# Kernel optimization log

Measured on AMD Instinct MI355X. Metric: run time of the kernel, lower is better.

Reference implementation:

```python
import jax, jax.numpy as jnp
import numpy as np

B, N, D = 2048, 128, 32   # samples, features, per-feature embed dim
H = 8                     # num_head
ND = N * D                # flattened width = 4096
U = D * N // H            # per-head units = 512
DH = D // H               # per-head output feature dim = 4


def setup_inputs() -> dict:
    key = jax.random.key(0)
    k_x, k_q, k_k, k_v, k_o = jax.random.split(key, 5)
    scale_w = 0.02  # keep QK^T logits in a sane range for softmax
    x = jax.random.normal(k_x, (B, N, D), dtype=jnp.float32)
    Wq = jax.random.normal(k_q, (H, ND, U), dtype=jnp.float32) * scale_w
    Wk = jax.random.normal(k_k, (H, ND, U), dtype=jnp.float32) * scale_w
    Wv = jax.random.normal(k_v, (H, ND, U), dtype=jnp.float32) * scale_w
    Wo = jax.random.normal(k_o, (D, D), dtype=jnp.float32) * (1.0 / np.sqrt(D))
    return {"x": x, "Wq": Wq, "Wk": Wk, "Wv": Wv, "Wo": Wo}


def reference(x, Wq, Wk, Wv, Wo):
    b, n, d = x.shape
    scale = d ** (-0.5)          # note: original scales by feature dim d, not head dim
    xf = x.reshape(b, n * d)     # (b, nd); the leading 1 axis in TF is vacuous
    # Batched per-head projections (collapses the Python head loop into one GEMM each)
    q = jnp.einsum('bf,hfu->hbu', xf, Wq)   # (H, b, U)
    k = jnp.einsum('bf,hfu->hbu', xf, Wk)   # (H, b, U)
    v = jnp.einsum('bf,hfu->hbu', xf, Wv)   # (H, b, U)
    scores = jax.nn.softmax(jnp.einsum('hbu,hcu->hbc', q, k) * scale, axis=-1)  # (H, b, b)
    av = jnp.einsum('hbc,hcu->hbu', scores, v)              # (H, b, U)
    # per-head reshape (b, U) -> (b, n, d/H), then concat heads along last dim
    av = av.reshape(H, b, n, d // H)                         # (H, b, n, dh)
    concat = jnp.transpose(av, (1, 2, 0, 3)).reshape(b, n, d)  # (b, n, d)
    return concat @ Wo  # dropout rate is 0 -> identity
```

## Files before the change

kernel.cpp:

```cpp
#include <hip/hip_runtime.h>
#include <stdint.h>
#include <math.h>

typedef short    s16x8 __attribute__((ext_vector_type(8)));
typedef float    f32x4 __attribute__((ext_vector_type(4)));
typedef uint32_t u32x4 __attribute__((ext_vector_type(4)));
typedef unsigned short u16x4 __attribute__((ext_vector_type(4)));

__device__ __forceinline__ uint16_t f2bf(float f) {
  union { float f; uint32_t u; } v; v.f = f;
  uint32_t r = v.u + 0x7fffu + ((v.u >> 16) & 1u);
  return (uint16_t)(r >> 16);
}
__device__ __forceinline__ float bf2f(uint16_t h) {
  union { uint32_t u; float f; } v; v.u = ((uint32_t)h) << 16;
  return v.f;
}

__device__ __forceinline__ void gld16(const void* g, void* l) {
  __builtin_amdgcn_global_load_lds(
      (const __attribute__((address_space(1))) void*)g,
      (__attribute__((address_space(3))) void*)l, 16, 0, 0);
}

__global__ __launch_bounds__(256) void cvt_x(const float* __restrict__ x,
                                             uint16_t* __restrict__ xf,
                                             float* __restrict__ rs) {
  if (blockIdx.x < 64) rs[blockIdx.x * 256 + threadIdx.x] = 0.f;
  size_t i = ((size_t)blockIdx.x * 256 + threadIdx.x) * 4;
  f32x4 v = *(const f32x4*)(x + i);
  u16x4 o = { f2bf(v.x), f2bf(v.y), f2bf(v.z), f2bf(v.w) };
  *(u16x4*)(xf + i) = o;
}

__global__ __launch_bounds__(256) void wtrans(const float* __restrict__ W0,
                                              const float* __restrict__ W1,
                                              const float* __restrict__ W2,
                                              uint16_t* __restrict__ Wt) {
  const int z = blockIdx.z;
  const float* W = (z < 8 ? W0 : (z < 16 ? W1 : W2)) + (size_t)(z & 7) * (4096 * 512);
  const int f0 = blockIdx.x * 32, u0 = blockIdx.y * 32;
  __shared__ float t[32][33];
  const int tid = threadIdx.x;
  {
    const int fi = tid >> 3, uu = (tid & 7) * 4;
    f32x4 v = *(const f32x4*)(W + (size_t)(f0 + fi) * 512 + u0 + uu);
    t[fi][uu] = v.x; t[fi][uu + 1] = v.y; t[fi][uu + 2] = v.z; t[fi][uu + 3] = v.w;
  }
  __syncthreads();
  {
    const int ui = tid >> 3, ff = (tid & 7) * 4;
    u16x4 o = { f2bf(t[ff][ui]), f2bf(t[ff + 1][ui]),
                f2bf(t[ff + 2][ui]), f2bf(t[ff + 3][ui]) };
    *(u16x4*)&Wt[((size_t)z * 512 + u0 + ui) * 4096 + f0 + ff] = o;
  }
}

template <int MODE>
__global__ __launch_bounds__(256, 4) void gemm_bt(
    const uint16_t* __restrict__ A, size_t sAz,
    const uint16_t* __restrict__ B, size_t sBz,
    void* __restrict__ C0, void* __restrict__ C1,
    int K, float scale, float* __restrict__ rs) {
  const int tid = threadIdx.x;
  const int wave = tid >> 6, lane = tid & 63;
  const int quad = lane >> 4, l16 = lane & 15;
  const int wrow = (wave >> 1) * 64, wcol = (wave & 1) * 64;
  const int m0 = blockIdx.y * 128, n0 = blockIdx.x * 128;
  const int z = blockIdx.z;
  A += (size_t)z * sAz;
  B += (size_t)z * sBz;

  __shared__ __align__(16) uint16_t lA[128 * 64];
  __shared__ __align__(16) uint16_t lB[128 * 64];

  f32x4 acc[4][4];
#pragma unroll
  for (int i = 0; i < 4; i++)
#pragma unroll
    for (int j = 0; j < 4; j++) acc[i][j] = f32x4{0.f, 0.f, 0.f, 0.f};

  const int lrow = lane >> 3;
  const int cs = ((lane & 7) ^ (lrow & 7)) * 8;
  const int rs0 = wave * 8;
  const uint16_t* gA = A + (size_t)(m0 + rs0 + lrow) * K + cs;
  const uint16_t* gB = B + (size_t)(n0 + rs0 + lrow) * K + cs;
  const size_t row32 = (size_t)32 * K;
  uint16_t* sA = &lA[rs0 * 64];
  uint16_t* sB = &lB[rs0 * 64];

  for (int k0 = 0; k0 < K; k0 += 64) {
    __syncthreads();
#pragma unroll
    for (int g = 0; g < 4; g++) {
      gld16(gA + g * row32, sA + g * 2048);
      gld16(gB + g * row32, sB + g * 2048);
    }
    gA += 64; gB += 64;
    __syncthreads();
#pragma unroll
    for (int h = 0; h < 2; h++) {
      s16x8 af[4], bfr[4];
      const int fsw = (((h * 4 + quad) ^ (l16 & 7)) * 8);
#pragma unroll
      for (int i = 0; i < 4; i++)
        af[i] = *(const s16x8*)&lA[(wrow + i * 16 + l16) * 64 + fsw];
#pragma unroll
      for (int j = 0; j < 4; j++)
        bfr[j] = *(const s16x8*)&lB[(wcol + j * 16 + l16) * 64 + fsw];
#pragma unroll
      for (int i = 0; i < 4; i++)
#pragma unroll
        for (int j = 0; j < 4; j++)
          acc[i][j] = __builtin_amdgcn_mfma_f32_16x16x32_bf16(af[i], bfr[j], acc[i][j], 0, 0, 0);
    }
  }

  const int mb = m0 + wrow + quad * 4;
  const int nb = n0 + wcol + l16;
  if (MODE == 4) {
    if (z < 16) {
      uint16_t* C = (uint16_t*)C0 + ((size_t)z << 20);
#pragma unroll
      for (int i = 0; i < 4; i++)
#pragma unroll
        for (int j = 0; j < 4; j++)
#pragma unroll
          for (int r = 0; r < 4; r++)
            C[(size_t)(mb + i * 16 + r) * 512 + (nb + j * 16)] = f2bf(acc[i][j][r]);
    } else {
      uint16_t* C = (uint16_t*)C1 + ((size_t)(z - 16) << 20);
#pragma unroll
      for (int i = 0; i < 4; i++)
#pragma unroll
        for (int j = 0; j < 4; j++) {
          u16x4 o = { f2bf(acc[i][j][0]), f2bf(acc[i][j][1]),
                      f2bf(acc[i][j][2]), f2bf(acc[i][j][3]) };
          *(u16x4*)&((uint16_t*)C)[(size_t)(nb + j * 16) * 2048 + (mb + i * 16)] = o;
        }
    }
  } else if (MODE == 2) {
    uint16_t* C = (uint16_t*)C0 + ((size_t)z << 22);
    float* rz = rs + (z << 11);
    float si[4][4];
#pragma unroll
    for (int i = 0; i < 4; i++)
#pragma unroll
      for (int r = 0; r < 4; r++) si[i][r] = 0.f;
#pragma unroll
    for (int i = 0; i < 4; i++)
#pragma unroll
      for (int j = 0; j < 4; j++)
#pragma unroll
        for (int r = 0; r < 4; r++) {
          float e = exp2f(fmaf(acc[i][j][r], scale, -43.2808512f));
          uint16_t hb = f2bf(e);
          C[(size_t)(mb + i * 16 + r) * 2048 + (nb + j * 16)] = hb;
          si[i][r] += bf2f(hb);
        }
#pragma unroll
    for (int i = 0; i < 4; i++)
#pragma unroll
      for (int r = 0; r < 4; r++) {
        float s = si[i][r];
        s += __shfl_xor(s, 1);
        s += __shfl_xor(s, 2);
        s += __shfl_xor(s, 4);
        s += __shfl_xor(s, 8);
        si[i][r] = s;
      }
    if (l16 == 0) {
#pragma unroll
      for (int i = 0; i < 4; i++)
#pragma unroll
        for (int r = 0; r < 4; r++)
          atomicAdd(&rz[mb + i * 16 + r], si[i][r]);
    }
  } else {
    float* C = (float*)C0 + ((size_t)z << 20);
    const float* rz = rs + (z << 11);
#pragma unroll
    for (int i = 0; i < 4; i++)
#pragma unroll
      for (int r = 0; r < 4; r++) {
        float w = 1.0f / rz[mb + i * 16 + r];
#pragma unroll
        for (int j = 0; j < 4; j++)
          C[(size_t)(mb + i * 16 + r) * 512 + (nb + j * 16)] = acc[i][j][r] * w;
      }
  }
}

__global__ __launch_bounds__(256) void out_proj(const float* __restrict__ av,
                                                const float* __restrict__ Wo,
                                                float* __restrict__ out) {
  __shared__ float lw[1024];
  const int tid = threadIdx.x;
#pragma unroll
  for (int i = 0; i < 4; i++) lw[tid + i * 256] = Wo[tid + i * 256];
  __syncthreads();
  const int p = blockIdx.x * 256 + tid;
  const int b = p >> 7, n = p & 127;
  float c[32];
#pragma unroll
  for (int h = 0; h < 8; h++) {
    f32x4 v = *(const f32x4*)(av + ((size_t)h * 2048 + b) * 512 + n * 4);
    c[h * 4] = v.x; c[h * 4 + 1] = v.y; c[h * 4 + 2] = v.z; c[h * 4 + 3] = v.w;
  }
  float o[32];
#pragma unroll
  for (int d = 0; d < 32; d++) o[d] = 0.f;
#pragma unroll
  for (int j = 0; j < 32; j++) {
    float cj = c[j];
#pragma unroll
    for (int d = 0; d < 32; d++) o[d] = fmaf(cj, lw[j * 32 + d], o[d]);
  }
  float* dst = out + (size_t)p * 32;
#pragma unroll
  for (int i = 0; i < 8; i++) {
    f32x4 v = { o[i * 4], o[i * 4 + 1], o[i * 4 + 2], o[i * 4 + 3] };
    *(f32x4*)(dst + i * 4) = v;
  }
}

extern "C" void kernel_launch(void* const* d_in, const int* in_sizes, int n_in,
                              void* d_out, int out_size, void* d_ws, size_t ws_size,
                              hipStream_t stream) {
  const float* x  = (const float*)d_in[0];
  const float* Wq = (const float*)d_in[1];
  const float* Wk = (const float*)d_in[2];
  const float* Wv = (const float*)d_in[3];
  const float* Wo = (const float*)d_in[4];
  float* out = (float*)d_out;

  uint8_t* ws = (uint8_t*)d_ws;
  uint16_t* Wt = (uint16_t*)(ws);
  uint16_t* P  = (uint16_t*)(ws);
  float*    av = (float*)(ws + 67108864);
  uint16_t* xf = (uint16_t*)(ws + 100663296);
  uint16_t* q  = (uint16_t*)(ws + 117440512);
  uint16_t* vt = (uint16_t*)(ws + 150994944);
  float*    rs = (float*)(ws + 167772160);

  const size_t WtH = (size_t)512 * 4096;
  const float scale2 = 0.17677669529663687f * 1.4426950408889634f;

  cvt_x<<<8192, 256, 0, stream>>>(x, xf, rs);
  wtrans<<<dim3(128, 16, 24), 256, 0, stream>>>(Wq, Wk, Wv, Wt);

  gemm_bt<4><<<dim3(4, 16, 24), 256, 0, stream>>>(
      xf, 0, Wt, WtH, q, vt, 4096, 0.f, nullptr);

  gemm_bt<2><<<dim3(16, 16, 8), 256, 0, stream>>>(
      q, (size_t)2048 * 512, q + (size_t)8 * 2048 * 512, (size_t)2048 * 512,
      P, nullptr, 512, scale2, rs);

  gemm_bt<3><<<dim3(4, 16, 8), 256, 0, stream>>>(
      P, (size_t)2048 * 2048, vt, (size_t)512 * 2048,
      av, nullptr, 2048, 0.f, rs);

  out_proj<<<1024, 256, 0, stream>>>(av, Wo, out);
}
```

Before: 572.1 us.

## Split-K the attention-value GEMM and widen weight transpose tiles

The P·V GEMM is split into two K halves across a doubled grid, and each half writes its own fp32 partial output. out_proj sums the two partials before the output projection. This raises block count and occupancy for a GEMM that previously launched too few blocks to fill the device, at the cost of an extra 32MB partial buffer read. The weight transpose kernel also processes 64x32 tiles with 8-wide bf16 stores to cut launch count and widen memory transactions.

Result: no change. 565.1 us (-1.2%).

```diff
diff --git a/kernel.cpp b/kernel.cpp
--- a/kernel.cpp
+++ b/kernel.cpp
@@ -6,6 +6,7 @@
 typedef float    f32x4 __attribute__((ext_vector_type(4)));
 typedef uint32_t u32x4 __attribute__((ext_vector_type(4)));
 typedef unsigned short u16x4 __attribute__((ext_vector_type(4)));
+typedef unsigned short u16x8 __attribute__((ext_vector_type(8)));
 
 __device__ __forceinline__ uint16_t f2bf(float f) {
   union { float f; uint32_t u; } v; v.f = f;
@@ -39,20 +40,24 @@
                                               uint16_t* __restrict__ Wt) {
   const int z = blockIdx.z;
   const float* W = (z < 8 ? W0 : (z < 16 ? W1 : W2)) + (size_t)(z & 7) * (4096 * 512);
-  const int f0 = blockIdx.x * 32, u0 = blockIdx.y * 32;
-  __shared__ float t[32][33];
+  const int f0 = blockIdx.x * 64, u0 = blockIdx.y * 32;
+  __shared__ float t[64][33];
   const int tid = threadIdx.x;
   {
-    const int fi = tid >> 3, uu = (tid & 7) * 4;
-    f32x4 v = *(const f32x4*)(W + (size_t)(f0 + fi) * 512 + u0 + uu);
-    t[fi][uu] = v.x; t[fi][uu + 1] = v.y; t[fi][uu + 2] = v.z; t[fi][uu + 3] = v.w;
+    const int fi = tid >> 2, uu = (tid & 3) * 8;
+    const float* src = W + (size_t)(f0 + fi) * 512 + u0 + uu;
+    f32x4 v0 = *(const f32x4*)src;
+    f32x4 v1 = *(const f32x4*)(src + 4);
+    t[fi][uu] = v0.x; t[fi][uu + 1] = v0.y; t[fi][uu + 2] = v0.z; t[fi][uu + 3] = v0.w;
+    t[fi][uu + 4] = v1.x; t[fi][uu + 5] = v1.y; t[fi][uu + 6] = v1.z; t[fi][uu + 7] = v1.w;
   }
   __syncthreads();
   {
-    const int ui = tid >> 3, ff = (tid & 7) * 4;
-    u16x4 o = { f2bf(t[ff][ui]), f2bf(t[ff + 1][ui]),
-                f2bf(t[ff + 2][ui]), f2bf(t[ff + 3][ui]) };
-    *(u16x4*)&Wt[((size_t)z * 512 + u0 + ui) * 4096 + f0 + ff] = o;
+    const int uo = tid >> 3, fo = (tid & 7) * 8;
+    u16x8 o = { f2bf(t[fo][uo]),     f2bf(t[fo + 1][uo]), f2bf(t[fo + 2][uo]),
+                f2bf(t[fo + 3][uo]), f2bf(t[fo + 4][uo]), f2bf(t[fo + 5][uo]),
+                f2bf(t[fo + 6][uo]), f2bf(t[fo + 7][uo]) };
+    *(u16x8*)&Wt[((size_t)z * 512 + u0 + uo) * 4096 + f0 + fo] = o;
   }
 }
 
@@ -67,9 +72,10 @@
   const int quad = lane >> 4, l16 = lane & 15;
   const int wrow = (wave >> 1) * 64, wcol = (wave & 1) * 64;
   const int m0 = blockIdx.y * 128, n0 = blockIdx.x * 128;
-  const int z = blockIdx.z;
-  A += (size_t)z * sAz;
-  B += (size_t)z * sBz;
+  int z = blockIdx.z, kh = 0, Kloop = K;
+  if (MODE == 3) { kh = z >> 3; z &= 7; Kloop = K >> 1; }
+  A += (size_t)z * sAz + (size_t)kh * Kloop;
+  B += (size_t)z * sBz + (size_t)kh * Kloop;
 
   __shared__ __align__(16) uint16_t lA[128 * 64];
   __shared__ __align__(16) uint16_t lB[128 * 64];
@@ -89,7 +95,7 @@
   uint16_t* sA = &lA[rs0 * 64];
   uint16_t* sB = &lB[rs0 * 64];
 
-  for (int k0 = 0; k0 < K; k0 += 64) {
+  for (int k0 = 0; k0 < Kloop; k0 += 64) {
     __syncthreads();
 #pragma unroll
     for (int g = 0; g < 4; g++) {
@@ -136,7 +142,7 @@
         for (int j = 0; j < 4; j++) {
           u16x4 o = { f2bf(acc[i][j][0]), f2bf(acc[i][j][1]),
                       f2bf(acc[i][j][2]), f2bf(acc[i][j][3]) };
-          *(u16x4*)&((uint16_t*)C)[(size_t)(nb + j * 16) * 2048 + (mb + i * 16)] = o;
+          *(u16x4*)&C[(size_t)(nb + j * 16) * 2048 + (mb + i * 16)] = o;
         }
     }
   } else if (MODE == 2) {
@@ -177,7 +183,7 @@
           atomicAdd(&rz[mb + i * 16 + r], si[i][r]);
     }
   } else {
-    float* C = (float*)C0 + ((size_t)z << 20);
+    float* C = (float*)(kh ? C1 : C0) + ((size_t)z << 20);
     const float* rz = rs + (z << 11);
 #pragma unroll
     for (int i = 0; i < 4; i++)
@@ -191,7 +197,8 @@
   }
 }
 
-__global__ __launch_bounds__(256) void out_proj(const float* __restrict__ av,
+__global__ __launch_bounds__(256) void out_proj(const float* __restrict__ av0,
+                                                const float* __restrict__ av1,
                                                 const float* __restrict__ Wo,
                                                 float* __restrict__ out) {
   __shared__ float lw[1024];
@@ -203,9 +210,12 @@
   const int b = p >> 7, n = p & 127;
   float c[32];
 #pragma unroll
-  for (int h = 0; h < 8; h++) {
-    f32x4 v = *(const f32x4*)(av + ((size_t)h * 2048 + b) * 512 + n * 4);
-    c[h * 4] = v.x; c[h * 4 + 1] = v.y; c[h * 4 + 2] = v.z; c[h * 4 + 3] = v.w;
+  for (int hh = 0; hh < 8; hh++) {
+    size_t idx = ((size_t)hh * 2048 + b) * 512 + n * 4;
+    f32x4 v = *(const f32x4*)(av0 + idx);
+    f32x4 w = *(const f32x4*)(av1 + idx);
+    c[hh * 4] = v.x + w.x; c[hh * 4 + 1] = v.y + w.y;
+    c[hh * 4 + 2] = v.z + w.z; c[hh * 4 + 3] = v.w + w.w;
   }
   float o[32];
 #pragma unroll
@@ -235,19 +245,20 @@
   float* out = (float*)d_out;
 
   uint8_t* ws = (uint8_t*)d_ws;
-  uint16_t* Wt = (uint16_t*)(ws);
-  uint16_t* P  = (uint16_t*)(ws);
-  float*    av = (float*)(ws + 67108864);
-  uint16_t* xf = (uint16_t*)(ws + 100663296);
-  uint16_t* q  = (uint16_t*)(ws + 117440512);
-  uint16_t* vt = (uint16_t*)(ws + 150994944);
-  float*    rs = (float*)(ws + 167772160);
+  uint16_t* Wt  = (uint16_t*)(ws);
+  uint16_t* P   = (uint16_t*)(ws);
+  float*    av0 = (float*)(ws + 67108864);
+  uint16_t* xf  = (uint16_t*)(ws + 100663296);
+  uint16_t* q   = (uint16_t*)(ws + 117440512);
+  float*    av1 = (float*)(ws + 117440512);
+  uint16_t* vt  = (uint16_t*)(ws + 150994944);
+  float*    rs  = (float*)(ws + 167772160);
 
   const size_t WtH = (size_t)512 * 4096;
   const float scale2 = 0.17677669529663687f * 1.4426950408889634f;
 
   cvt_x<<<8192, 256, 0, stream>>>(x, xf, rs);
-  wtrans<<<dim3(128, 16, 24), 256, 0, stream>>>(Wq, Wk, Wv, Wt);
+  wtrans<<<dim3(64, 16, 24), 256, 0, stream>>>(Wq, Wk, Wv, Wt);
 
   gemm_bt<4><<<dim3(4, 16, 24), 256, 0, stream>>>(
       xf, 0, Wt, WtH, q, vt, 4096, 0.f, nullptr);
@@ -256,9 +267,9 @@
       q, (size_t)2048 * 512, q + (size_t)8 * 2048 * 512, (size_t)2048 * 512,
       P, nullptr, 512, scale2, rs);
 
-  gemm_bt<3><<<dim3(4, 16, 8), 256, 0, stream>>>(
+  gemm_bt<3><<<dim3(4, 16, 16), 256, 0, stream>>>(
       P, (size_t)2048 * 2048, vt, (size_t)512 * 2048,
-      av, nullptr, 2048, 0.f, rs);
-
-  out_proj<<<1024, 256, 0, stream>>>(av, Wo, out);
-}
+      av0, av1, 2048, 0.f, rs);
+
+  out_proj<<<1024, 256, 0, stream>>>(av0, av1, Wo, out);
+}
```
